# Kernel tuning notes

Measured on AMD Instinct MI355X. Metric: run time of the kernel, lower is better.

## Reference

```python
import jax, jax.numpy as jnp
import numpy as np

MARGIN = 0.5
LOSS_WEIGHT = 1.0
EPS_NORM = 1e-10


def setup_inputs() -> dict:
    key = jax.random.key(0)
    k1, k2 = jax.random.split(key)
    pred = jax.random.normal(k1, (512, 512), dtype=jnp.float32)
    target = jax.random.randint(k2, (512,), 0, 2, dtype=jnp.int32)
    return {"pred": pred, "target": target}


def reference(pred, target):
    bs = pred.shape[0]
    # F.normalize(pred, eps=1e-10): L2-normalize rows
    norm = jnp.linalg.norm(pred, axis=1, keepdims=True)
    p = pred / jnp.maximum(norm, EPS_NORM)
    sq = jnp.sum(p * p, axis=1)  # [bs]
    d2 = -2.0 * (p @ p.T) + sq[:, None] + sq[None, :]
    d2 = jnp.maximum(d2, 0.0)  # dist[dist < 0] = 0
    # safe sqrt (forward identical to torch.sqrt on clamped d2)
    pos = d2 > 0
    dist = jnp.sqrt(jnp.where(pos, d2, 1.0)) * pos.astype(d2.dtype)  # [bs, bs]

    target_ = 1.0 - target.astype(jnp.float32)
    broad = target_[:, None] + target_[None, :]  # [bs, bs]
    not_eye = 1.0 - jnp.eye(bs, dtype=jnp.float32)
    pp = not_eye * (broad == 0.0).astype(jnp.float32)  # anchor-positive mask [bs, bs]
    pn = not_eye * (broad == 1.0).astype(jnp.float32)  # anchor-negative mask [bs, bs]

    # loss[i,j,k] = dist[i,j] - dist[i,k] + margin, masked by pp[i,j] * pn[j,k]
    loss = dist[:, :, None] - dist[:, None, :] + MARGIN  # [bs, bs, bs]
    apn = pp[:, :, None] * pn[None, :, :]  # [bs, bs, bs]
    loss = jnp.maximum(loss * apn, 0.0)  # loss[loss < 0] = 0
    num_tri = jnp.sum((loss > 0.0).astype(jnp.float32))
    total = jnp.sum(loss) * LOSS_WEIGHT
    return total / (num_tri + 1e-7)
```

## Files before the change

### kernel.cpp

```cpp
#include <hip/hip_runtime.h>
#include <hip/hip_bf16.h>

#define BS 512
#define MARGIN 0.5f

using short8 = __attribute__((ext_vector_type(8))) short;
using f32x4 = __attribute__((ext_vector_type(4))) float;

__device__ inline short bf16_rne(float x) {
    __hip_bfloat16 h = __float2bfloat16(x);
    return *(short*)&h;
}

__global__ __launch_bounds__(64) void kdistf(const float* __restrict__ pred,
                                             const int* __restrict__ target,
                                             float* __restrict__ dist,
                                             int* __restrict__ counts) {
    const int lane = threadIdx.x;
    __shared__ int plist[BS];
    __shared__ int rnk[BS];
    __shared__ int tgs[BS];

    int pbase = 0, nbase = 0;
    const unsigned long long below = (1ULL << lane) - 1ULL;
#pragma unroll
    for (int c = 0; c < 8; ++c) {
        const int idx = c * 64 + lane;
        const int tg = target[idx];
        const unsigned long long mp = __ballot(tg == 1);
        const int prk = pbase + __popcll(mp & below);
        const int nrk = nbase + __popcll((~mp) & below);
        tgs[idx] = tg;
        rnk[idx] = (tg == 1) ? prk : nrk;
        if (tg == 1) plist[prk] = idx;
        const int np = __popcll(mp);
        pbase += np;
        nbase += 64 - np;
    }
    const int npos = pbase;
    __syncthreads();

    if (blockIdx.x == 0 && blockIdx.y == 0 && lane == 0) {
        counts[0] = npos;
        counts[1] = nbase;
    }

    const int r0 = blockIdx.y * 32;
    if (r0 >= npos) return;
    const int c0 = blockIdx.x * 32;
    const int rl = lane & 15;
    const int koff = (lane >> 4) * 8;

    const int pr0 = min(r0 + rl, npos - 1);
    const int pr1 = min(r0 + 16 + rl, npos - 1);
    const float* A0 = pred + plist[pr0] * BS;
    const float* A1 = pred + plist[pr1] * BS;
    const float* B0 = pred + (c0 + rl) * BS;
    const float* B1 = pred + (c0 + 16 + rl) * BS;

    f32x4 acc00 = {0.f, 0.f, 0.f, 0.f};
    f32x4 acc01 = {0.f, 0.f, 0.f, 0.f};
    f32x4 acc10 = {0.f, 0.f, 0.f, 0.f};
    f32x4 acc11 = {0.f, 0.f, 0.f, 0.f};
    float na0 = 0.f, na1 = 0.f, nb0 = 0.f, nb1 = 0.f;

#pragma unroll 4
    for (int ks = 0; ks < 16; ++ks) {
        const int k = ks * 32 + koff;
        const f32x4 a0l = *(const f32x4*)(A0 + k);
        const f32x4 a0h = *(const f32x4*)(A0 + k + 4);
        const f32x4 a1l = *(const f32x4*)(A1 + k);
        const f32x4 a1h = *(const f32x4*)(A1 + k + 4);
        const f32x4 b0l = *(const f32x4*)(B0 + k);
        const f32x4 b0h = *(const f32x4*)(B0 + k + 4);
        const f32x4 b1l = *(const f32x4*)(B1 + k);
        const f32x4 b1h = *(const f32x4*)(B1 + k + 4);

        short8 sa0, sa1, sb0, sb1;
#pragma unroll
        for (int j = 0; j < 4; ++j) {
            na0 += a0l[j] * a0l[j] + a0h[j] * a0h[j];
            na1 += a1l[j] * a1l[j] + a1h[j] * a1h[j];
            nb0 += b0l[j] * b0l[j] + b0h[j] * b0h[j];
            nb1 += b1l[j] * b1l[j] + b1h[j] * b1h[j];
            sa0[j] = bf16_rne(a0l[j]); sa0[4 + j] = bf16_rne(a0h[j]);
            sa1[j] = bf16_rne(a1l[j]); sa1[4 + j] = bf16_rne(a1h[j]);
            sb0[j] = bf16_rne(b0l[j]); sb0[4 + j] = bf16_rne(b0h[j]);
            sb1[j] = bf16_rne(b1l[j]); sb1[4 + j] = bf16_rne(b1h[j]);
        }
        acc00 = __builtin_amdgcn_mfma_f32_16x16x32_bf16(sa0, sb0, acc00, 0, 0, 0);
        acc01 = __builtin_amdgcn_mfma_f32_16x16x32_bf16(sa0, sb1, acc01, 0, 0, 0);
        acc10 = __builtin_amdgcn_mfma_f32_16x16x32_bf16(sa1, sb0, acc10, 0, 0, 0);
        acc11 = __builtin_amdgcn_mfma_f32_16x16x32_bf16(sa1, sb1, acc11, 0, 0, 0);
    }

    na0 += __shfl_xor(na0, 16, 64); na0 += __shfl_xor(na0, 32, 64);
    na1 += __shfl_xor(na1, 16, 64); na1 += __shfl_xor(na1, 32, 64);
    nb0 += __shfl_xor(nb0, 16, 64); nb0 += __shfl_xor(nb0, 32, 64);
    nb1 += __shfl_xor(nb1, 16, 64); nb1 += __shfl_xor(nb1, 32, 64);
    const float ia0 = 1.0f / fmaxf(sqrtf(na0), 1e-10f);
    const float ia1 = 1.0f / fmaxf(sqrtf(na1), 1e-10f);
    const float ib0 = 1.0f / fmaxf(sqrtf(nb0), 1e-10f);
    const float ib1 = 1.0f / fmaxf(sqrtf(nb1), 1e-10f);

    const int rbase = (lane >> 4) * 4;
#pragma unroll
    for (int fr = 0; fr < 2; ++fr) {
        const float iaSel = (fr == 0) ? ia0 : ia1;
#pragma unroll
        for (int fc = 0; fc < 2; ++fc) {
            f32x4 v = (fr == 0) ? (fc == 0 ? acc00 : acc01) : (fc == 0 ? acc10 : acc11);
            const int col = c0 + fc * 16 + rl;
            const float icol = (fc == 0) ? ib0 : ib1;
            const int isPos = tgs[col];
            const int ccol = (isPos == 1) ? rnk[col] : npos + rnk[col];
            const float addM = (isPos == 1) ? MARGIN : 0.0f;
#pragma unroll
            for (int r = 0; r < 4; ++r) {
                const float irow = __shfl(iaSel, rbase + r, 64);
                const int rowp = r0 + fr * 16 + rbase + r;
                float d2 = 2.0f - 2.0f * v[r] * irow * icol;
                dist[rowp * BS + ccol] = sqrtf(fmaxf(d2, 0.f)) + addM;
            }
        }
    }
}

__global__ __launch_bounds__(256) void ktriplet(const float* __restrict__ dist,
                                                const int* __restrict__ counts,
                                                float* __restrict__ psum,
                                                float* __restrict__ pcnt) {
    const int b = blockIdx.x;
    const int tid = threadIdx.x;
    const int npos = counts[0];
    if (b >= npos) {
        if (tid == 0) { psum[b] = 0.f; pcnt[b] = 0.f; }
        return;
    }
    const int nneg = counts[1];
    const int lane = tid & 63;
    const int w = tid >> 6;
    __shared__ float sbuf[4];
    __shared__ float cbuf[4];

    const float* drow = dist + b * BS;

    const float bv0 = (tid < nneg) ? drow[npos + tid] : 1e30f;
    const float bv1 = (tid + 256 < nneg) ? drow[npos + 256 + tid] : 1e30f;

    const int ja = w * 64 + lane;
    const int jb = (w + 4) * 64 + lane;
    const float av0 = (ja < npos && ja != b) ? drow[ja] : -1e9f;
    const float av1 = (jb < npos && jb != b) ? drow[jb] : -1e9f;

    float sum = 0.f;
    unsigned int cw = 0;

#define HINGE(TJ, BK)                                       \
    do {                                                    \
        const float v_ = (TJ) - (BK);                       \
        sum += fmaxf(v_, 0.f);                              \
        cw += (unsigned int)__popcll(__ballot(v_ > 0.f));   \
    } while (0)

    if (nneg > 256) {
        if (w * 64 < npos) {
#pragma unroll 8
            for (int jj = 0; jj < 64; ++jj) {
                const float tj = __int_as_float(
                    __builtin_amdgcn_readlane(__float_as_int(av0), jj));
                HINGE(tj, bv0); HINGE(tj, bv1);
            }
        }
        if ((w + 4) * 64 < npos) {
#pragma unroll 8
            for (int jj = 0; jj < 64; ++jj) {
                const float tj = __int_as_float(
                    __builtin_amdgcn_readlane(__float_as_int(av1), jj));
                HINGE(tj, bv0); HINGE(tj, bv1);
            }
        }
    } else {
        if (w * 64 < npos) {
#pragma unroll 8
            for (int jj = 0; jj < 64; ++jj) {
                const float tj = __int_as_float(
                    __builtin_amdgcn_readlane(__float_as_int(av0), jj));
                HINGE(tj, bv0);
            }
        }
        if ((w + 4) * 64 < npos) {
#pragma unroll 8
            for (int jj = 0; jj < 64; ++jj) {
                const float tj = __int_as_float(
                    __builtin_amdgcn_readlane(__float_as_int(av1), jj));
                HINGE(tj, bv0);
            }
        }
    }
#undef HINGE

    float wsm = sum;
#pragma unroll
    for (int o = 32; o > 0; o >>= 1) wsm += __shfl_xor(wsm, o, 64);
    if (lane == 0) { sbuf[w] = wsm; cbuf[w] = (float)cw; }
    __syncthreads();
    if (tid == 0) {
        psum[b] = (sbuf[0] + sbuf[1]) + (sbuf[2] + sbuf[3]);
        pcnt[b] = (cbuf[0] + cbuf[1]) + (cbuf[2] + cbuf[3]);
    }
}

__global__ __launch_bounds__(64) void kfinal(const float* __restrict__ psum,
                                             const float* __restrict__ pcnt,
                                             float* __restrict__ out) {
    const int lane = threadIdx.x;
    float s = 0.f, c = 0.f;
#pragma unroll
    for (int r = 0; r < 8; ++r) {
        s += psum[r * 64 + lane];
        c += pcnt[r * 64 + lane];
    }
#pragma unroll
    for (int o = 32; o > 0; o >>= 1) {
        s += __shfl_xor(s, o, 64);
        c += __shfl_xor(c, o, 64);
    }
    if (lane == 0) out[0] = s / (c + 1e-7f);
}

extern "C" void kernel_launch(void* const* d_in, const int* in_sizes, int n_in,
                              void* d_out, int out_size, void* d_ws, size_t ws_size,
                              hipStream_t stream) {
    const float* pred = (const float*)d_in[0];
    const int* target = (const int*)d_in[1];
    float* out = (float*)d_out;
    char* base = (char*)d_ws;

    float* dist = (float*)base;
    float* psum = (float*)(base + 1048576);
    float* pcnt = (float*)(base + 1050624);
    int* counts = (int*)(base + 1052672);

    dim3 gb(16, 16);
    kdistf<<<gb, 64, 0, stream>>>(pred, target, dist, counts);
    ktriplet<<<512, 256, 0, stream>>>(dist, counts, psum, pcnt);
    kfinal<<<1, 64, 0, stream>>>(psum, pcnt, out);
}
```

Baseline: 22.03 us.

## Fuse final reduction into triplet kernel and halve distance row tiles

The separate single-block final reduction kernel is removed. The last ktriplet block to finish, found through an atomic counter with threadfences, now sums the per-row partials, saving one kernel launch. The distance kernel tiles 16 rows per block instead of 32 and launches twice as many blocks to raise parallelism on the small matrix, at the cost of reloading the B tiles more often. ktriplet blocks with no work now fall through to the counter logic instead of returning early.

```diff
diff --git a/kernel.cpp b/kernel.cpp
--- a/kernel.cpp
+++ b/kernel.cpp
@@ -3,6 +3,7 @@
 
 #define BS 512
 #define MARGIN 0.5f
+#define NBLK 512
 
 using short8 = __attribute__((ext_vector_type(8))) short;
 using f32x4 = __attribute__((ext_vector_type(4))) float;
@@ -15,7 +16,8 @@
 __global__ __launch_bounds__(64) void kdistf(const float* __restrict__ pred,
                                              const int* __restrict__ target,
                                              float* __restrict__ dist,
-                                             int* __restrict__ counts) {
+                                             int* __restrict__ counts,
+                                             unsigned int* __restrict__ fin) {
     const int lane = threadIdx.x;
     __shared__ int plist[BS];
     __shared__ int rnk[BS];
@@ -43,82 +45,69 @@
     if (blockIdx.x == 0 && blockIdx.y == 0 && lane == 0) {
         counts[0] = npos;
         counts[1] = nbase;
-    }
-
-    const int r0 = blockIdx.y * 32;
+        *fin = 0u;
+    }
+
+    const int r0 = blockIdx.y * 16;
     if (r0 >= npos) return;
     const int c0 = blockIdx.x * 32;
     const int rl = lane & 15;
     const int koff = (lane >> 4) * 8;
 
-    const int pr0 = min(r0 + rl, npos - 1);
-    const int pr1 = min(r0 + 16 + rl, npos - 1);
-    const float* A0 = pred + plist[pr0] * BS;
-    const float* A1 = pred + plist[pr1] * BS;
+    const int pr = min(r0 + rl, npos - 1);
+    const float* A = pred + plist[pr] * BS;
     const float* B0 = pred + (c0 + rl) * BS;
     const float* B1 = pred + (c0 + 16 + rl) * BS;
 
-    f32x4 acc00 = {0.f, 0.f, 0.f, 0.f};
-    f32x4 acc01 = {0.f, 0.f, 0.f, 0.f};
-    f32x4 acc10 = {0.f, 0.f, 0.f, 0.f};
-    f32x4 acc11 = {0.f, 0.f, 0.f, 0.f};
-    float na0 = 0.f, na1 = 0.f, nb0 = 0.f, nb1 = 0.f;
+    f32x4 acc0 = {0.f, 0.f, 0.f, 0.f};
+    f32x4 acc1 = {0.f, 0.f, 0.f, 0.f};
+    float na = 0.f, nb0 = 0.f, nb1 = 0.f;
 
 #pragma unroll 4
     for (int ks = 0; ks < 16; ++ks) {
         const int k = ks * 32 + koff;
-        const f32x4 a0l = *(const f32x4*)(A0 + k);
-        const f32x4 a0h = *(const f32x4*)(A0 + k + 4);
-        const f32x4 a1l = *(const f32x4*)(A1 + k);
-        const f32x4 a1h = *(const f32x4*)(A1 + k + 4);
+        const f32x4 al = *(const f32x4*)(A + k);
+        const f32x4 ah = *(const f32x4*)(A + k + 4);
         const f32x4 b0l = *(const f32x4*)(B0 + k);
         const f32x4 b0h = *(const f32x4*)(B0 + k + 4);
         const f32x4 b1l = *(const f32x4*)(B1 + k);
         const f32x4 b1h = *(const f32x4*)(B1 + k + 4);
 
-        short8 sa0, sa1, sb0, sb1;
+        short8 sa, sb0, sb1;
 #pragma unroll
         for (int j = 0; j < 4; ++j) {
-            na0 += a0l[j] * a0l[j] + a0h[j] * a0h[j];
-            na1 += a1l[j] * a1l[j] + a1h[j] * a1h[j];
+            na += al[j] * al[j] + ah[j] * ah[j];
             nb0 += b0l[j] * b0l[j] + b0h[j] * b0h[j];
             nb1 += b1l[j] * b1l[j] + b1h[j] * b1h[j];
-            sa0[j] = bf16_rne(a0l[j]); sa0[4 + j] = bf16_rne(a0h[j]);
-            sa1[j] = bf16_rne(a1l[j]); sa1[4 + j] = bf16_rne(a1h[j]);
+            sa[j] = bf16_rne(al[j]);  sa[4 + j] = bf16_rne(ah[j]);
             sb0[j] = bf16_rne(b0l[j]); sb0[4 + j] = bf16_rne(b0h[j]);
             sb1[j] = bf16_rne(b1l[j]); sb1[4 + j] = bf16_rne(b1h[j]);
         }
-        acc00 = __builtin_amdgcn_mfma_f32_16x16x32_bf16(sa0, sb0, acc00, 0, 0, 0);
-        acc01 = __builtin_amdgcn_mfma_f32_16x16x32_bf16(sa0, sb1, acc01, 0, 0, 0);
-        acc10 = __builtin_amdgcn_mfma_f32_16x16x32_bf16(sa1, sb0, acc10, 0, 0, 0);
-        acc11 = __builtin_amdgcn_mfma_f32_16x16x32_bf16(sa1, sb1, acc11, 0, 0, 0);
-    }
-
-    na0 += __shfl_xor(na0, 16, 64); na0 += __shfl_xor(na0, 32, 64);
-    na1 += __shfl_xor(na1, 16, 64); na1 += __shfl_xor(na1, 32, 64);
+        acc0 = __builtin_amdgcn_mfma_f32_16x16x32_bf16(sa, sb0, acc0, 0, 0, 0);
+        acc1 = __builtin_amdgcn_mfma_f32_16x16x32_bf16(sa, sb1, acc1, 0, 0, 0);
+    }
+
+    na += __shfl_xor(na, 16, 64); na += __shfl_xor(na, 32, 64);
     nb0 += __shfl_xor(nb0, 16, 64); nb0 += __shfl_xor(nb0, 32, 64);
     nb1 += __shfl_xor(nb1, 16, 64); nb1 += __shfl_xor(nb1, 32, 64);
-    const float ia0 = 1.0f / fmaxf(sqrtf(na0), 1e-10f);
-    const float ia1 = 1.0f / fmaxf(sqrtf(na1), 1e-10f);
+    const float ia = 1.0f / fmaxf(sqrtf(na), 1e-10f);
     const float ib0 = 1.0f / fmaxf(sqrtf(nb0), 1e-10f);
     const float ib1 = 1.0f / fmaxf(sqrtf(nb1), 1e-10f);
 
     const int rbase = (lane >> 4) * 4;
 #pragma unroll
-    for (int fr = 0; fr < 2; ++fr) {
-        const float iaSel = (fr == 0) ? ia0 : ia1;
-#pragma unroll
-        for (int fc = 0; fc < 2; ++fc) {
-            f32x4 v = (fr == 0) ? (fc == 0 ? acc00 : acc01) : (fc == 0 ? acc10 : acc11);
-            const int col = c0 + fc * 16 + rl;
-            const float icol = (fc == 0) ? ib0 : ib1;
-            const int isPos = tgs[col];
-            const int ccol = (isPos == 1) ? rnk[col] : npos + rnk[col];
-            const float addM = (isPos == 1) ? MARGIN : 0.0f;
-#pragma unroll
-            for (int r = 0; r < 4; ++r) {
-                const float irow = __shfl(iaSel, rbase + r, 64);
-                const int rowp = r0 + fr * 16 + rbase + r;
+    for (int fc = 0; fc < 2; ++fc) {
+        const f32x4 v = (fc == 0) ? acc0 : acc1;
+        const int col = c0 + fc * 16 + rl;
+        const float icol = (fc == 0) ? ib0 : ib1;
+        const int isPos = tgs[col];
+        const int ccol = (isPos == 1) ? rnk[col] : npos + rnk[col];
+        const float addM = (isPos == 1) ? MARGIN : 0.0f;
+#pragma unroll
+        for (int r = 0; r < 4; ++r) {
+            const float irow = __shfl(ia, rbase + r, 64);
+            const int rowp = r0 + rbase + r;
+            if (rowp < npos) {
                 float d2 = 2.0f - 2.0f * v[r] * irow * icol;
                 dist[rowp * BS + ccol] = sqrtf(fmaxf(d2, 0.f)) + addM;
             }
@@ -129,32 +118,32 @@
 __global__ __launch_bounds__(256) void ktriplet(const float* __restrict__ dist,
                                                 const int* __restrict__ counts,
                                                 float* __restrict__ psum,
-                                                float* __restrict__ pcnt) {
+                                                float* __restrict__ pcnt,
+                                                unsigned int* __restrict__ fin,
+                                                float* __restrict__ out) {
     const int b = blockIdx.x;
     const int tid = threadIdx.x;
-    const int npos = counts[0];
-    if (b >= npos) {
-        if (tid == 0) { psum[b] = 0.f; pcnt[b] = 0.f; }
-        return;
-    }
-    const int nneg = counts[1];
     const int lane = tid & 63;
     const int w = tid >> 6;
+    const int npos = counts[0];
+    const int nneg = counts[1];
     __shared__ float sbuf[4];
     __shared__ float cbuf[4];
-
-    const float* drow = dist + b * BS;
-
-    const float bv0 = (tid < nneg) ? drow[npos + tid] : 1e30f;
-    const float bv1 = (tid + 256 < nneg) ? drow[npos + 256 + tid] : 1e30f;
-
-    const int ja = w * 64 + lane;
-    const int jb = (w + 4) * 64 + lane;
-    const float av0 = (ja < npos && ja != b) ? drow[ja] : -1e9f;
-    const float av1 = (jb < npos && jb != b) ? drow[jb] : -1e9f;
+    __shared__ unsigned int slast;
 
     float sum = 0.f;
     unsigned int cw = 0;
+
+    if (b < npos) {
+        const float* drow = dist + b * BS;
+
+        const float bv0 = (tid < nneg) ? drow[npos + tid] : 1e30f;
+        const float bv1 = (tid + 256 < nneg) ? drow[npos + 256 + tid] : 1e30f;
+
+        const int ja = w * 64 + lane;
+        const int jb = (w + 4) * 64 + lane;
+        const float av0 = (ja < npos && ja != b) ? drow[ja] : -1e9f;
+        const float av1 = (jb < npos && jb != b) ? drow[jb] : -1e9f;
 
 #define HINGE(TJ, BK)                                       \
     do {                                                    \
@@ -163,42 +152,43 @@
         cw += (unsigned int)__popcll(__ballot(v_ > 0.f));   \
     } while (0)
 
-    if (nneg > 256) {
-        if (w * 64 < npos) {
-#pragma unroll 8
-            for (int jj = 0; jj < 64; ++jj) {
-                const float tj = __int_as_float(
-                    __builtin_amdgcn_readlane(__float_as_int(av0), jj));
-                HINGE(tj, bv0); HINGE(tj, bv1);
-            }
-        }
-        if ((w + 4) * 64 < npos) {
-#pragma unroll 8
-            for (int jj = 0; jj < 64; ++jj) {
-                const float tj = __int_as_float(
-                    __builtin_amdgcn_readlane(__float_as_int(av1), jj));
-                HINGE(tj, bv0); HINGE(tj, bv1);
-            }
-        }
-    } else {
-        if (w * 64 < npos) {
-#pragma unroll 8
-            for (int jj = 0; jj < 64; ++jj) {
-                const float tj = __int_as_float(
-                    __builtin_amdgcn_readlane(__float_as_int(av0), jj));
-                HINGE(tj, bv0);
-            }
-        }
-        if ((w + 4) * 64 < npos) {
-#pragma unroll 8
-            for (int jj = 0; jj < 64; ++jj) {
-                const float tj = __int_as_float(
-                    __builtin_amdgcn_readlane(__float_as_int(av1), jj));
-                HINGE(tj, bv0);
-            }
-        }
-    }
+        if (nneg > 256) {
+            if (w * 64 < npos) {
+#pragma unroll 8
+                for (int jj = 0; jj < 64; ++jj) {
+                    const float tj = __int_as_float(
+                        __builtin_amdgcn_readlane(__float_as_int(av0), jj));
+                    HINGE(tj, bv0); HINGE(tj, bv1);
+                }
+            }
+            if ((w + 4) * 64 < npos) {
+#pragma unroll 8
+                for (int jj = 0; jj < 64; ++jj) {
+                    const float tj = __int_as_float(
+                        __builtin_amdgcn_readlane(__float_as_int(av1), jj));
+                    HINGE(tj, bv0); HINGE(tj, bv1);
+                }
+            }
+        } else {
+            if (w * 64 < npos) {
+#pragma unroll 8
+                for (int jj = 0; jj < 64; ++jj) {
+                    const float tj = __int_as_float(
+                        __builtin_amdgcn_readlane(__float_as_int(av0), jj));
+                    HINGE(tj, bv0);
+                }
+            }
+            if ((w + 4) * 64 < npos) {
+#pragma unroll 8
+                for (int jj = 0; jj < 64; ++jj) {
+                    const float tj = __int_as_float(
+                        __builtin_amdgcn_readlane(__float_as_int(av1), jj));
+                    HINGE(tj, bv0);
+                }
+            }
+        }
 #undef HINGE
+    }
 
     float wsm = sum;
 #pragma unroll
@@ -208,25 +198,25 @@
     if (tid == 0) {
         psum[b] = (sbuf[0] + sbuf[1]) + (sbuf[2] + sbuf[3]);
         pcnt[b] = (cbuf[0] + cbuf[1]) + (cbuf[2] + cbuf[3]);
-    }
-}
-
-__global__ __launch_bounds__(64) void kfinal(const float* __restrict__ psum,
-                                             const float* __restrict__ pcnt,
-                                             float* __restrict__ out) {
-    const int lane = threadIdx.x;
-    float s = 0.f, c = 0.f;
-#pragma unroll
-    for (int r = 0; r < 8; ++r) {
-        s += psum[r * 64 + lane];
-        c += pcnt[r * 64 + lane];
-    }
-#pragma unroll
-    for (int o = 32; o > 0; o >>= 1) {
-        s += __shfl_xor(s, o, 64);
-        c += __shfl_xor(c, o, 64);
-    }
-    if (lane == 0) out[0] = s / (c + 1e-7f);
+        __threadfence();
+        slast = (atomicAdd(fin, 1u) == (unsigned int)(NBLK - 1)) ? 1u : 0u;
+    }
+    __syncthreads();
+    if (slast != 0 && tid < 64) {
+        __threadfence();
+        float s = 0.f, c = 0.f;
+#pragma unroll
+        for (int r = 0; r < 8; ++r) {
+            s += psum[r * 64 + tid];
+            c += pcnt[r * 64 + tid];
+        }
+#pragma unroll
+        for (int o = 32; o > 0; o >>= 1) {
+            s += __shfl_xor(s, o, 64);
+            c += __shfl_xor(c, o, 64);
+        }
+        if (tid == 0) out[0] = s / (c + 1e-7f);
+    }
 }
 
 extern "C" void kernel_launch(void* const* d_in, const int* in_sizes, int n_in,
@@ -241,9 +231,9 @@
     float* psum = (float*)(base + 1048576);
     float* pcnt = (float*)(base + 1050624);
     int* counts = (int*)(base + 1052672);
-
-    dim3 gb(16, 16);
-    kdistf<<<gb, 64, 0, stream>>>(pred, target, dist, counts);
-    ktriplet<<<512, 256, 0, stream>>>(dist, counts, psum, pcnt);
-    kfinal<<<1, 64, 0, stream>>>(psum, pcnt, out);
-}
+    unsigned int* fin = (unsigned int*)(base + 1052736);
+
+    dim3 gb(16, 32);
+    kdistf<<<gb, 64, 0, stream>>>(pred, target, dist, counts, fin);
+    ktriplet<<<NBLK, 256, 0, stream>>>(dist, counts, psum, pcnt, fin, out);
+}
```

After: 26.74 us. 21.4% more time.

## Split the Gram matrix K dimension across two blocks and finish distances in the triplet kernel

Applied to the files above, without the earlier changes.

The distance kernel now splits the 512-wide inner dimension into two halves via blockIdx.z. Each half writes partial dot products and partial squared norms to separate planes, doubling the number of blocks on the GPU. The triplet kernel sums the two partials and computes the normalization, sqrt and margin on the fly. This exposes more parallelism in the small first kernel. In exchange it doubles intermediate memory traffic and moves per-element sqrt/reciprocal work into the triplet kernel's load phase.

```diff
diff --git a/kernel.cpp b/kernel.cpp
--- a/kernel.cpp
+++ b/kernel.cpp
@@ -3,6 +3,7 @@
 
 #define BS 512
 #define MARGIN 0.5f
+#define PLANE 262144
 
 using short8 = __attribute__((ext_vector_type(8))) short;
 using f32x4 = __attribute__((ext_vector_type(4))) float;
@@ -12,11 +13,14 @@
     return *(short*)&h;
 }
 
-__global__ __launch_bounds__(64) void kdistf(const float* __restrict__ pred,
+__global__ __launch_bounds__(64) void kdistp(const float* __restrict__ pred,
                                              const int* __restrict__ target,
-                                             float* __restrict__ dist,
+                                             float* __restrict__ pdot,
+                                             float* __restrict__ nrmA,
+                                             float* __restrict__ nrmC,
                                              int* __restrict__ counts) {
     const int lane = threadIdx.x;
+    const int kh = blockIdx.z;
     __shared__ int plist[BS];
     __shared__ int rnk[BS];
     __shared__ int tgs[BS];
@@ -40,7 +44,7 @@
     const int npos = pbase;
     __syncthreads();
 
-    if (blockIdx.x == 0 && blockIdx.y == 0 && lane == 0) {
+    if (blockIdx.x == 0 && blockIdx.y == 0 && kh == 0 && lane == 0) {
         counts[0] = npos;
         counts[1] = nbase;
     }
@@ -50,13 +54,14 @@
     const int c0 = blockIdx.x * 32;
     const int rl = lane & 15;
     const int koff = (lane >> 4) * 8;
+    const int kbase = kh * 256;
 
     const int pr0 = min(r0 + rl, npos - 1);
     const int pr1 = min(r0 + 16 + rl, npos - 1);
-    const float* A0 = pred + plist[pr0] * BS;
-    const float* A1 = pred + plist[pr1] * BS;
-    const float* B0 = pred + (c0 + rl) * BS;
-    const float* B1 = pred + (c0 + 16 + rl) * BS;
+    const float* A0 = pred + plist[pr0] * BS + kbase;
+    const float* A1 = pred + plist[pr1] * BS + kbase;
+    const float* B0 = pred + (c0 + rl) * BS + kbase;
+    const float* B1 = pred + (c0 + 16 + rl) * BS + kbase;
 
     f32x4 acc00 = {0.f, 0.f, 0.f, 0.f};
     f32x4 acc01 = {0.f, 0.f, 0.f, 0.f};
@@ -65,7 +70,7 @@
     float na0 = 0.f, na1 = 0.f, nb0 = 0.f, nb1 = 0.f;
 
 #pragma unroll 4
-    for (int ks = 0; ks < 16; ++ks) {
+    for (int ks = 0; ks < 8; ++ks) {
         const int k = ks * 32 + koff;
         const f32x4 a0l = *(const f32x4*)(A0 + k);
         const f32x4 a0h = *(const f32x4*)(A0 + k + 4);
@@ -98,35 +103,42 @@
     na1 += __shfl_xor(na1, 16, 64); na1 += __shfl_xor(na1, 32, 64);
     nb0 += __shfl_xor(nb0, 16, 64); nb0 += __shfl_xor(nb0, 32, 64);
     nb1 += __shfl_xor(nb1, 16, 64); nb1 += __shfl_xor(nb1, 32, 64);
-    const float ia0 = 1.0f / fmaxf(sqrtf(na0), 1e-10f);
-    const float ia1 = 1.0f / fmaxf(sqrtf(na1), 1e-10f);
-    const float ib0 = 1.0f / fmaxf(sqrtf(nb0), 1e-10f);
-    const float ib1 = 1.0f / fmaxf(sqrtf(nb1), 1e-10f);
+
+    float* pd = pdot + kh * PLANE;
+    float* nA = nrmA + kh * 512;
+    float* nC = nrmC + kh * 512;
+
+    if (lane < 16) {
+        nA[r0 + lane] = na0;
+        nA[r0 + 16 + lane] = na1;
+        const int ca = c0 + lane;
+        const int cca = (tgs[ca] == 1) ? rnk[ca] : npos + rnk[ca];
+        nC[cca] = nb0;
+        const int cb = c0 + 16 + lane;
+        const int ccb = (tgs[cb] == 1) ? rnk[cb] : npos + rnk[cb];
+        nC[ccb] = nb1;
+    }
 
     const int rbase = (lane >> 4) * 4;
 #pragma unroll
     for (int fr = 0; fr < 2; ++fr) {
-        const float iaSel = (fr == 0) ? ia0 : ia1;
 #pragma unroll
         for (int fc = 0; fc < 2; ++fc) {
             f32x4 v = (fr == 0) ? (fc == 0 ? acc00 : acc01) : (fc == 0 ? acc10 : acc11);
             const int col = c0 + fc * 16 + rl;
-            const float icol = (fc == 0) ? ib0 : ib1;
-            const int isPos = tgs[col];
-            const int ccol = (isPos == 1) ? rnk[col] : npos + rnk[col];
-            const float addM = (isPos == 1) ? MARGIN : 0.0f;
+            const int ccol = (tgs[col] == 1) ? rnk[col] : npos + rnk[col];
 #pragma unroll
             for (int r = 0; r < 4; ++r) {
-                const float irow = __shfl(iaSel, rbase + r, 64);
                 const int rowp = r0 + fr * 16 + rbase + r;
-                float d2 = 2.0f - 2.0f * v[r] * irow * icol;
-                dist[rowp * BS + ccol] = sqrtf(fmaxf(d2, 0.f)) + addM;
-            }
-        }
-    }
-}
-
-__global__ __launch_bounds__(256) void ktriplet(const float* __restrict__ dist,
+                pd[rowp * BS + ccol] = v[r];
+            }
+        }
+    }
+}
+
+__global__ __launch_bounds__(256) void ktriplet(const float* __restrict__ pdot,
+                                                const float* __restrict__ nrmA,
+                                                const float* __restrict__ nrmC,
                                                 const int* __restrict__ counts,
                                                 float* __restrict__ psum,
                                                 float* __restrict__ pcnt) {
@@ -143,15 +155,25 @@
     __shared__ float sbuf[4];
     __shared__ float cbuf[4];
 
-    const float* drow = dist + b * BS;
-
-    const float bv0 = (tid < nneg) ? drow[npos + tid] : 1e30f;
-    const float bv1 = (tid + 256 < nneg) ? drow[npos + 256 + tid] : 1e30f;
+    const float* d0 = pdot + b * BS;
+    const float* d1 = pdot + PLANE + b * BS;
+    const float nAb = nrmA[b] + nrmA[512 + b];
+    const float ia = 1.0f / fmaxf(sqrtf(nAb), 1e-10f);
+
+    auto dcol = [&](int cc) -> float {
+        const float dot = d0[cc] + d1[cc];
+        const float nc = nrmC[cc] + nrmC[512 + cc];
+        const float ic = 1.0f / fmaxf(sqrtf(nc), 1e-10f);
+        return sqrtf(fmaxf(2.0f - 2.0f * dot * ia * ic, 0.0f));
+    };
+
+    const float bv0 = (tid < nneg) ? dcol(npos + tid) : 1e30f;
+    const float bv1 = (tid + 256 < nneg) ? dcol(npos + 256 + tid) : 1e30f;
 
     const int ja = w * 64 + lane;
     const int jb = (w + 4) * 64 + lane;
-    const float av0 = (ja < npos && ja != b) ? drow[ja] : -1e9f;
-    const float av1 = (jb < npos && jb != b) ? drow[jb] : -1e9f;
+    const float av0 = (ja < npos && ja != b) ? dcol(ja) + MARGIN : -1e9f;
+    const float av1 = (jb < npos && jb != b) ? dcol(jb) + MARGIN : -1e9f;
 
     float sum = 0.f;
     unsigned int cw = 0;
@@ -237,13 +259,15 @@
     float* out = (float*)d_out;
     char* base = (char*)d_ws;
 
-    float* dist = (float*)base;
-    float* psum = (float*)(base + 1048576);
-    float* pcnt = (float*)(base + 1050624);
-    int* counts = (int*)(base + 1052672);
-
-    dim3 gb(16, 16);
-    kdistf<<<gb, 64, 0, stream>>>(pred, target, dist, counts);
-    ktriplet<<<512, 256, 0, stream>>>(dist, counts, psum, pcnt);
+    float* pdot = (float*)base;
+    float* nrmA = (float*)(base + 2097152);
+    float* nrmC = (float*)(base + 2101248);
+    float* psum = (float*)(base + 2105344);
+    float* pcnt = (float*)(base + 2107392);
+    int* counts = (int*)(base + 2109440);
+
+    dim3 gb(16, 16, 2);
+    kdistp<<<gb, 64, 0, stream>>>(pred, target, pdot, nrmA, nrmC, counts);
+    ktriplet<<<512, 256, 0, stream>>>(pdot, nrmA, nrmC, counts, psum, pcnt);
     kfinal<<<1, 64, 0, stream>>>(psum, pcnt, out);
 }
```

Measured after the change: 19.92 us (median of 2 runs). 9.6% less time.
